# Performance work log

Measured on AMD Instinct MI355X. Metric: run time of the kernel, lower is better.

Reference implementation:

```python
import jax, jax.numpy as jnp
import numpy as np

B, T, F, H = 4096, 512, 16, 256
OUTPUT_LEN = 64


def setup_inputs() -> dict:
    key = jax.random.key(0)
    ks = jax.random.split(key, 9)
    s = 1.0 / np.sqrt(H)  # pytorch LSTM default init scale
    return {
        "x": jax.random.normal(ks[0], (B, T, F), jnp.float32),
        # encoder LSTM (single layer). b = b_ih + b_hh combined.
        "enc_Wih": jax.random.uniform(ks[1], (4 * H, F), jnp.float32, -s, s),
        "enc_Whh": jax.random.uniform(ks[2], (4 * H, H), jnp.float32, -s, s),
        "enc_b": jax.random.uniform(ks[3], (4 * H,), jnp.float32, -s, s),
        # decoder LSTM, input size 1
        "dec_Wih": jax.random.uniform(ks[4], (4 * H, 1), jnp.float32, -s, s),
        "dec_Whh": jax.random.uniform(ks[5], (4 * H, H), jnp.float32, -s, s),
        "dec_b": jax.random.uniform(ks[6], (4 * H,), jnp.float32, -s, s),
        # output head Linear(H, 1)
        "Wout": jax.random.uniform(ks[7], (1, H), jnp.float32, -s, s),
        "bout": jax.random.uniform(ks[8], (1,), jnp.float32, -s, s),
    }


def _lstm_cell(h, c, x_t, Wih, Whh, b):
    # PyTorch gate order: i, f, g, o
    gates = x_t @ Wih.T + h @ Whh.T + b  # [B, 4H]
    i, f, g, o = jnp.split(gates, 4, axis=-1)
    c = jax.nn.sigmoid(f) * c + jax.nn.sigmoid(i) * jnp.tanh(g)
    h = jax.nn.sigmoid(o) * jnp.tanh(c)
    return h, c


def reference(x, enc_Wih, enc_Whh, enc_b, dec_Wih, dec_Whh, dec_b, Wout, bout):
    Bb = x.shape[0]
    Hh = enc_Whh.shape[1]
    h0 = jnp.zeros((Bb, Hh), x.dtype)
    c0 = jnp.zeros((Bb, Hh), x.dtype)

    def enc_step(carry, x_t):
        h, c = carry
        h, c = _lstm_cell(h, c, x_t, enc_Wih, enc_Whh, enc_b)
        return (h, c), None

    (h, c), _ = jax.lax.scan(enc_step, (h0, c0), jnp.swapaxes(x, 0, 1))

    def dec_step(carry, _):
        h, c, inp = carry  # inp: [B, 1]
        h, c = _lstm_cell(h, c, inp, dec_Wih, dec_Whh, dec_b)
        # dropout is identity in eval mode
        out = h @ Wout.T + bout  # [B, 1]
        return (h, c, out), out

    inp0 = jnp.zeros((Bb, 1), x.dtype)
    _, outs = jax.lax.scan(dec_step, (h, c, inp0), None, length=OUTPUT_LEN)
    # outs: [output_len, B, 1] -> [B, output_len, 1]
    return jnp.swapaxes(outs, 0, 1)
```

## Files before the change

### kernel.cpp

```cpp
#include <hip/hip_runtime.h>

#define TT 512
#define FF 16
#define HH 256
#define OUTLEN 64
#define NT 9
#define PITCH 296
#define ROWS 16
#define NBLK (4096/ROWS)
#define NFRAG (NT*16*4*64)

typedef _Float16 half8 __attribute__((ext_vector_type(8)));
typedef float f32x4 __attribute__((ext_vector_type(4)));

__device__ __forceinline__ float fsig(float x) {
  return __builtin_amdgcn_rcpf(1.0f + __expf(-x));
}
__device__ __forceinline__ float ftanh(float x) { return 2.0f * fsig(x + x) - 1.0f; }

__global__ void prep_kernel(const float* __restrict__ eWih, const float* __restrict__ eWhh,
                            const float* __restrict__ eb,  const float* __restrict__ dWih,
                            const float* __restrict__ dWhh, const float* __restrict__ db,
                            _Float16* __restrict__ E, _Float16* __restrict__ D) {
  int idx = blockIdx.x * 256 + threadIdx.x;
  if (idx >= NFRAG * 8) return;
  int j    = idx & 7;
  int lane = (idx >> 3) & 63;
  int rest = idx >> 9;
  int g    = rest & 3;
  int wv   = (rest >> 2) & 15;
  int kt   = rest >> 6;
  int col  = g * 256 + wv * 16 + (lane & 15);
  int k    = kt * 32 + (lane >> 4) * 8 + j;
  float ve = 0.f, vd = 0.f;
  if (k < HH)        { ve = eWhh[col * HH + k]; vd = dWhh[col * HH + k]; }
  else if (k == HH)  { ve = eb[col];            vd = db[col]; }
  else if (k <= 272) { ve = eWih[col * FF + (k - 257)]; if (k == 257) vd = dWih[col]; }
  E[idx] = (_Float16)ve;
  D[idx] = (_Float16)vd;
}

__device__ __forceinline__ void fill_bf(half8 (&bf)[2][4], const half8* __restrict__ strm) {
#pragma unroll
  for (int g = 0; g < 4; ++g) bf[0][g] = strm[0 * 4096 + g * 64];
#pragma unroll
  for (int g = 0; g < 4; ++g) bf[1][g] = strm[1 * 4096 + g * 64];
}

__device__ __forceinline__ void fill_pk(half8 (&pk)[3][4], const half8* __restrict__ pp) {
#pragma unroll
  for (int i = 0; i < 3; ++i)
#pragma unroll
    for (int g = 0; g < 4; ++g) pk[i][g] = pp[i * 4096 + g * 64];
}

#define PIN_PK(pk)                                                   \
  _Pragma("unroll")                                                  \
  for (int _i = 0; _i < 3; ++_i)                                     \
    _Pragma("unroll")                                                \
    for (int _g = 0; _g < 4; ++_g)                                   \
      asm volatile("" : "+v"(pk[_i][_g]));

__device__ __forceinline__ void mfma_step(const _Float16* __restrict__ uHp,
                                          const _Float16* __restrict__ uLp,
                                          const half8* __restrict__ Btp,
                                          const half8* __restrict__ strm,
                                          const half8 (&pk)[3][4],
                                          half8 (&bf)[2][4],
                                          f32x4 (&acc)[4]) {
#pragma unroll
  for (int g = 0; g < 4; ++g) acc[g] = (f32x4){0.f, 0.f, 0.f, 0.f};

#pragma unroll
  for (int s = 0; s < 2; ++s) {
    half8 AH = *(const half8*)(uHp + (5 + s) * 32);
    half8 AL = *(const half8*)(uLp + (5 + s) * 32);
#pragma unroll
    for (int g = 0; g < 4; ++g) acc[g] = __builtin_amdgcn_mfma_f32_16x16x32_f16(AH, bf[s][g], acc[g], 0, 0, 0);
#pragma unroll
    for (int g = 0; g < 4; ++g) acc[g] = __builtin_amdgcn_mfma_f32_16x16x32_f16(AL, bf[s][g], acc[g], 0, 0, 0);
    {
      const half8* rp = strm + (s + 2) * 4096;
#pragma unroll
      for (int g = 0; g < 4; ++g) bf[s][g] = rp[g * 64];
    }
  }

#pragma unroll
  for (int kt = 0; kt < 2; ++kt) {
    half8 b[4];
#pragma unroll
    for (int g = 0; g < 4; ++g) b[g] = Btp[kt * 4096 + g * 64];
    half8 AH = *(const half8*)(uHp + kt * 32);
    half8 AL = *(const half8*)(uLp + kt * 32);
#pragma unroll
    for (int g = 0; g < 4; ++g) acc[g] = __builtin_amdgcn_mfma_f32_16x16x32_f16(AH, b[g], acc[g], 0, 0, 0);
#pragma unroll
    for (int g = 0; g < 4; ++g) acc[g] = __builtin_amdgcn_mfma_f32_16x16x32_f16(AL, b[g], acc[g], 0, 0, 0);
  }

#pragma unroll
  for (int s = 2; s < 4; ++s) {
    half8 AH = *(const half8*)(uHp + (5 + s) * 32);
    half8 AL = *(const half8*)(uLp + (5 + s) * 32);
#pragma unroll
    for (int g = 0; g < 4; ++g) acc[g] = __builtin_amdgcn_mfma_f32_16x16x32_f16(AH, bf[s - 2][g], acc[g], 0, 0, 0);
#pragma unroll
    for (int g = 0; g < 4; ++g) acc[g] = __builtin_amdgcn_mfma_f32_16x16x32_f16(AL, bf[s - 2][g], acc[g], 0, 0, 0);
    {
      const half8* rp = strm + (s - 2) * 4096;
#pragma unroll
      for (int g = 0; g < 4; ++g) bf[s - 2][g] = rp[g * 64];
    }
  }

#pragma unroll
  for (int i = 0; i < 3; ++i) {
    half8 AH = *(const half8*)(uHp + (2 + i) * 32);
    half8 AL = *(const half8*)(uLp + (2 + i) * 32);
#pragma unroll
    for (int g = 0; g < 4; ++g) acc[g] = __builtin_amdgcn_mfma_f32_16x16x32_f16(AH, pk[i][g], acc[g], 0, 0, 0);
#pragma unroll
    for (int g = 0; g < 4; ++g) acc[g] = __builtin_amdgcn_mfma_f32_16x16x32_f16(AL, pk[i][g], acc[g], 0, 0, 0);
  }
}

__global__ __launch_bounds__(1024, 4) void seq2seq_kernel(
    const float* __restrict__ x,
    const _Float16* __restrict__ E, const _Float16* __restrict__ Dw,
    const float* __restrict__ Wout, const float* __restrict__ bout,
    float* __restrict__ out) {
  __shared__ _Float16 uH[ROWS * PITCH];
  __shared__ _Float16 uL[ROWS * PITCH];
  __shared__ half8 Bt[2 * 16 * 4 * 64];
  __shared__ float red[ROWS * 16];

  const int tid  = threadIdx.x;
  const int w    = tid >> 6;
  const int lane = tid & 63;
  const int quad = lane >> 4;
  const int l15  = lane & 15;
  const int b0   = blockIdx.x * ROWS;
  const int unit = w * 16 + l15;

  const half8* E8 = (const half8*)E;
  const half8* D8 = (const half8*)Dw;

  for (int i = tid; i < ROWS * PITCH; i += 1024) { uH[i] = (_Float16)0.f; uL[i] = (_Float16)0.f; }
  for (int i = tid; i < 8192; i += 1024) Bt[i] = E8[i];
  __syncthreads();
  if (tid < ROWS) uH[tid * PITCH + 256] = (_Float16)1.0f;

  const _Float16* uHp = uH + l15 * PITCH + quad * 8;
  const _Float16* uLp = uL + l15 * PITCH + quad * 8;
  const half8* Btp  = Bt + w * 256 + lane;
  const half8* strm = E8 + 5 * 4096 + w * 256 + lane;

  float cc[4] = {0.f, 0.f, 0.f, 0.f};
  const float wou = Wout[unit];
  const float bo  = bout[0];
  const int   xr  = (tid >> 4) * PITCH + 257 + (tid & 15);
  const float* xp = x + ((long)(b0 + (tid >> 4)) * TT) * FF + (tid & 15);

  half8 pk[3][4];
  fill_pk(pk, E8 + 2 * 4096 + w * 256 + lane);
  half8 bf[2][4];
  fill_bf(bf, strm);

  float xv = (tid < 256) ? xp[0] : 0.f;
#pragma unroll 1
  for (int t = 0; t < TT; ++t) {
    PIN_PK(pk);
    if (tid < 256) {
      _Float16 hs = (_Float16)xv;
      uH[xr] = hs; uL[xr] = (_Float16)(xv - (float)hs);
      if (t + 1 < TT) xv = xp[(t + 1) * FF];
    }
    __syncthreads();

    f32x4 acc[4];
    mfma_step(uHp, uLp, Btp, strm, pk, bf, acc);
    __syncthreads();

#pragma unroll
    for (int rg = 0; rg < 4; ++rg) {
      float ig = fsig(acc[0][rg]);
      float fg = fsig(acc[1][rg]);
      float gg = ftanh(acc[2][rg]);
      float og = fsig(acc[3][rg]);
      cc[rg] = fg * cc[rg] + ig * gg;
      float hv = og * ftanh(cc[rg]);
      const int m = quad * 4 + rg;
      _Float16 hs = (_Float16)hv;
      uH[m * PITCH + unit] = hs;
      uL[m * PITCH + unit] = (_Float16)(hv - (float)hs);
    }
  }

  __syncthreads();
  for (int i = tid; i < 8192; i += 1024) Bt[i] = D8[i];
  strm = D8 + 5 * 4096 + w * 256 + lane;
  fill_pk(pk, D8 + 2 * 4096 + w * 256 + lane);
  fill_bf(bf, strm);
  if (tid < ROWS) { uH[tid * PITCH + 257] = (_Float16)0.f; uL[tid * PITCH + 257] = (_Float16)0.f; }

#pragma unroll 1
  for (int td = 0; td < OUTLEN; ++td) {
    PIN_PK(pk);
    __syncthreads();

    f32x4 acc[4];
    mfma_step(uHp, uLp, Btp, strm, pk, bf, acc);
    __syncthreads();

    float p[4];
#pragma unroll
    for (int rg = 0; rg < 4; ++rg) {
      float ig = fsig(acc[0][rg]);
      float fg = fsig(acc[1][rg]);
      float gg = ftanh(acc[2][rg]);
      float og = fsig(acc[3][rg]);
      cc[rg] = fg * cc[rg] + ig * gg;
      float hv = og * ftanh(cc[rg]);
      const int m = quad * 4 + rg;
      _Float16 hs = (_Float16)hv;
      uH[m * PITCH + unit] = hs;
      uL[m * PITCH + unit] = (_Float16)(hv - (float)hs);
      p[rg] = hv * wou;
    }
#pragma unroll
    for (int off = 1; off < 16; off <<= 1)
#pragma unroll
      for (int rg = 0; rg < 4; ++rg) p[rg] += __shfl_xor(p[rg], off, 64);
    if (l15 == 0) {
#pragma unroll
      for (int rg = 0; rg < 4; ++rg) red[(quad * 4 + rg) * 16 + w] = p[rg];
    }
    __syncthreads();
    if (tid < ROWS) {
      float s = bo;
#pragma unroll
      for (int u = 0; u < 16; ++u) s += red[tid * 16 + u];
      out[(long)(b0 + tid) * OUTLEN + td] = s;
      _Float16 hs = (_Float16)s;
      uH[tid * PITCH + 257] = hs;
      uL[tid * PITCH + 257] = (_Float16)(s - (float)hs);
    }
  }
}

extern "C" void kernel_launch(void* const* d_in, const int* in_sizes, int n_in,
                              void* d_out, int out_size, void* d_ws, size_t ws_size,
                              hipStream_t stream) {
  const float* x    = (const float*)d_in[0];
  const float* eWih = (const float*)d_in[1];
  const float* eWhh = (const float*)d_in[2];
  const float* eb   = (const float*)d_in[3];
  const float* dWih = (const float*)d_in[4];
  const float* dWhh = (const float*)d_in[5];
  const float* db   = (const float*)d_in[6];
  const float* Wout = (const float*)d_in[7];
  const float* bout = (const float*)d_in[8];
  float* out = (float*)d_out;

  _Float16* E  = (_Float16*)d_ws;
  _Float16* Dw = E + NFRAG * 8;

  prep_kernel<<<dim3((NFRAG * 8 + 255) / 256), dim3(256), 0, stream>>>(
      eWih, eWhh, eb, dWih, dWhh, db, E, Dw);
  seq2seq_kernel<<<dim3(NBLK), dim3(1024), 0, stream>>>(
      x, E, Dw, Wout, bout, out);
}
```

Measured before the change: 2.899 ms.

## Halve block to 512 threads with each wave computing two hidden-unit slices

Each block now runs 8 waves instead of 16, and each wave owns two 16-unit column slices. A-fragment loads from LDS are reused across twice as many MFMAs, and the pinned weight fragments double per wave. The weight-streaming schedule is reorganised around consume/refill helpers. This cuts barrier participants and shared-memory A traffic but raises register pressure and halves thread-level parallelism per block, with launch bounds changed to (512,2).

```diff
diff --git a/kernel.cpp b/kernel.cpp
--- a/kernel.cpp
+++ b/kernel.cpp
@@ -40,92 +40,103 @@
   D[idx] = (_Float16)vd;
 }
 
-__device__ __forceinline__ void fill_bf(half8 (&bf)[2][4], const half8* __restrict__ strm) {
-#pragma unroll
-  for (int g = 0; g < 4; ++g) bf[0][g] = strm[0 * 4096 + g * 64];
-#pragma unroll
-  for (int g = 0; g < 4; ++g) bf[1][g] = strm[1 * 4096 + g * 64];
-}
-
-__device__ __forceinline__ void fill_pk(half8 (&pk)[3][4], const half8* __restrict__ pp) {
+__device__ __forceinline__ void refill_bf(half8 (&bf)[2][4], const half8* __restrict__ rp) {
+#pragma unroll
+  for (int s = 0; s < 2; ++s)
+#pragma unroll
+    for (int g = 0; g < 4; ++g) bf[s][g] = rp[s * 256 + g * 64];
+}
+
+__device__ __forceinline__ void fill_pk(half8 (&pk)[3][2][4], const half8* __restrict__ pp) {
 #pragma unroll
   for (int i = 0; i < 3; ++i)
 #pragma unroll
-    for (int g = 0; g < 4; ++g) pk[i][g] = pp[i * 4096 + g * 64];
+    for (int s = 0; s < 2; ++s)
+#pragma unroll
+      for (int g = 0; g < 4; ++g) pk[i][s][g] = pp[i * 4096 + s * 256 + g * 64];
 }
 
 #define PIN_PK(pk)                                                   \
   _Pragma("unroll")                                                  \
   for (int _i = 0; _i < 3; ++_i)                                     \
     _Pragma("unroll")                                                \
-    for (int _g = 0; _g < 4; ++_g)                                   \
-      asm volatile("" : "+v"(pk[_i][_g]));
+    for (int _s = 0; _s < 2; ++_s)                                   \
+      _Pragma("unroll")                                              \
+      for (int _g = 0; _g < 4; ++_g)                                 \
+        asm volatile("" : "+v"(pk[_i][_s][_g]));
+
+__device__ __forceinline__ void consume_bf(const _Float16* __restrict__ uHp,
+                                           const _Float16* __restrict__ uLp,
+                                           const int kt, const half8 (&bf)[2][4],
+                                           f32x4 (&acc)[2][4]) {
+  half8 AH = *(const half8*)(uHp + kt * 32);
+  half8 AL = *(const half8*)(uLp + kt * 32);
+#pragma unroll
+  for (int s = 0; s < 2; ++s) {
+#pragma unroll
+    for (int g = 0; g < 4; ++g) acc[s][g] = __builtin_amdgcn_mfma_f32_16x16x32_f16(AH, bf[s][g], acc[s][g], 0, 0, 0);
+#pragma unroll
+    for (int g = 0; g < 4; ++g) acc[s][g] = __builtin_amdgcn_mfma_f32_16x16x32_f16(AL, bf[s][g], acc[s][g], 0, 0, 0);
+  }
+}
+
+__device__ __forceinline__ void consume_lds(const _Float16* __restrict__ uHp,
+                                            const _Float16* __restrict__ uLp,
+                                            const int kt, const half8* __restrict__ Btp,
+                                            f32x4 (&acc)[2][4]) {
+  half8 AH = *(const half8*)(uHp + kt * 32);
+  half8 AL = *(const half8*)(uLp + kt * 32);
+#pragma unroll
+  for (int s = 0; s < 2; ++s) {
+    half8 b[4];
+#pragma unroll
+    for (int g = 0; g < 4; ++g) b[g] = Btp[kt * 4096 + s * 256 + g * 64];
+#pragma unroll
+    for (int g = 0; g < 4; ++g) acc[s][g] = __builtin_amdgcn_mfma_f32_16x16x32_f16(AH, b[g], acc[s][g], 0, 0, 0);
+#pragma unroll
+    for (int g = 0; g < 4; ++g) acc[s][g] = __builtin_amdgcn_mfma_f32_16x16x32_f16(AL, b[g], acc[s][g], 0, 0, 0);
+  }
+}
+
+__device__ __forceinline__ void consume_pin(const _Float16* __restrict__ uHp,
+                                            const _Float16* __restrict__ uLp,
+                                            const int i, const half8 (&pk)[3][2][4],
+                                            f32x4 (&acc)[2][4]) {
+  half8 AH = *(const half8*)(uHp + (2 + i) * 32);
+  half8 AL = *(const half8*)(uLp + (2 + i) * 32);
+#pragma unroll
+  for (int s = 0; s < 2; ++s) {
+#pragma unroll
+    for (int g = 0; g < 4; ++g) acc[s][g] = __builtin_amdgcn_mfma_f32_16x16x32_f16(AH, pk[i][s][g], acc[s][g], 0, 0, 0);
+#pragma unroll
+    for (int g = 0; g < 4; ++g) acc[s][g] = __builtin_amdgcn_mfma_f32_16x16x32_f16(AL, pk[i][s][g], acc[s][g], 0, 0, 0);
+  }
+}
 
 __device__ __forceinline__ void mfma_step(const _Float16* __restrict__ uHp,
                                           const _Float16* __restrict__ uLp,
                                           const half8* __restrict__ Btp,
                                           const half8* __restrict__ strm,
-                                          const half8 (&pk)[3][4],
+                                          const half8 (&pk)[3][2][4],
                                           half8 (&bf)[2][4],
-                                          f32x4 (&acc)[4]) {
-#pragma unroll
-  for (int g = 0; g < 4; ++g) acc[g] = (f32x4){0.f, 0.f, 0.f, 0.f};
-
-#pragma unroll
-  for (int s = 0; s < 2; ++s) {
-    half8 AH = *(const half8*)(uHp + (5 + s) * 32);
-    half8 AL = *(const half8*)(uLp + (5 + s) * 32);
-#pragma unroll
-    for (int g = 0; g < 4; ++g) acc[g] = __builtin_amdgcn_mfma_f32_16x16x32_f16(AH, bf[s][g], acc[g], 0, 0, 0);
-#pragma unroll
-    for (int g = 0; g < 4; ++g) acc[g] = __builtin_amdgcn_mfma_f32_16x16x32_f16(AL, bf[s][g], acc[g], 0, 0, 0);
-    {
-      const half8* rp = strm + (s + 2) * 4096;
-#pragma unroll
-      for (int g = 0; g < 4; ++g) bf[s][g] = rp[g * 64];
-    }
-  }
-
-#pragma unroll
-  for (int kt = 0; kt < 2; ++kt) {
-    half8 b[4];
-#pragma unroll
-    for (int g = 0; g < 4; ++g) b[g] = Btp[kt * 4096 + g * 64];
-    half8 AH = *(const half8*)(uHp + kt * 32);
-    half8 AL = *(const half8*)(uLp + kt * 32);
-#pragma unroll
-    for (int g = 0; g < 4; ++g) acc[g] = __builtin_amdgcn_mfma_f32_16x16x32_f16(AH, b[g], acc[g], 0, 0, 0);
-#pragma unroll
-    for (int g = 0; g < 4; ++g) acc[g] = __builtin_amdgcn_mfma_f32_16x16x32_f16(AL, b[g], acc[g], 0, 0, 0);
-  }
-
-#pragma unroll
-  for (int s = 2; s < 4; ++s) {
-    half8 AH = *(const half8*)(uHp + (5 + s) * 32);
-    half8 AL = *(const half8*)(uLp + (5 + s) * 32);
-#pragma unroll
-    for (int g = 0; g < 4; ++g) acc[g] = __builtin_amdgcn_mfma_f32_16x16x32_f16(AH, bf[s - 2][g], acc[g], 0, 0, 0);
-#pragma unroll
-    for (int g = 0; g < 4; ++g) acc[g] = __builtin_amdgcn_mfma_f32_16x16x32_f16(AL, bf[s - 2][g], acc[g], 0, 0, 0);
-    {
-      const half8* rp = strm + (s - 2) * 4096;
-#pragma unroll
-      for (int g = 0; g < 4; ++g) bf[s - 2][g] = rp[g * 64];
-    }
-  }
-
-#pragma unroll
-  for (int i = 0; i < 3; ++i) {
-    half8 AH = *(const half8*)(uHp + (2 + i) * 32);
-    half8 AL = *(const half8*)(uLp + (2 + i) * 32);
-#pragma unroll
-    for (int g = 0; g < 4; ++g) acc[g] = __builtin_amdgcn_mfma_f32_16x16x32_f16(AH, pk[i][g], acc[g], 0, 0, 0);
-#pragma unroll
-    for (int g = 0; g < 4; ++g) acc[g] = __builtin_amdgcn_mfma_f32_16x16x32_f16(AL, pk[i][g], acc[g], 0, 0, 0);
-  }
-}
-
-__global__ __launch_bounds__(1024, 4) void seq2seq_kernel(
+                                          f32x4 (&acc)[2][4]) {
+#pragma unroll
+  for (int s = 0; s < 2; ++s)
+#pragma unroll
+    for (int g = 0; g < 4; ++g) acc[s][g] = (f32x4){0.f, 0.f, 0.f, 0.f};
+
+  consume_bf(uHp, uLp, 5, bf, acc);  refill_bf(bf, strm + 1 * 4096);
+  consume_lds(uHp, uLp, 0, Btp, acc);
+  consume_bf(uHp, uLp, 6, bf, acc);  refill_bf(bf, strm + 2 * 4096);
+  consume_lds(uHp, uLp, 1, Btp, acc);
+  consume_bf(uHp, uLp, 7, bf, acc);  refill_bf(bf, strm + 3 * 4096);
+  consume_pin(uHp, uLp, 0, pk, acc);
+  consume_pin(uHp, uLp, 1, pk, acc);
+  consume_bf(uHp, uLp, 8, bf, acc);  refill_bf(bf, strm);
+  consume_pin(uHp, uLp, 2, pk, acc);
+}
+
+__global__ __launch_bounds__(512, 2) void seq2seq_kernel(
     const float* __restrict__ x,
     const _Float16* __restrict__ E, const _Float16* __restrict__ Dw,
     const float* __restrict__ Wout, const float* __restrict__ bout,
@@ -141,31 +152,32 @@
   const int quad = lane >> 4;
   const int l15  = lane & 15;
   const int b0   = blockIdx.x * ROWS;
-  const int unit = w * 16 + l15;
 
   const half8* E8 = (const half8*)E;
   const half8* D8 = (const half8*)Dw;
 
-  for (int i = tid; i < ROWS * PITCH; i += 1024) { uH[i] = (_Float16)0.f; uL[i] = (_Float16)0.f; }
-  for (int i = tid; i < 8192; i += 1024) Bt[i] = E8[i];
+  for (int i = tid; i < ROWS * PITCH; i += 512) { uH[i] = (_Float16)0.f; uL[i] = (_Float16)0.f; }
+  for (int i = tid; i < 8192; i += 512) Bt[i] = E8[i];
   __syncthreads();
   if (tid < ROWS) uH[tid * PITCH + 256] = (_Float16)1.0f;
 
   const _Float16* uHp = uH + l15 * PITCH + quad * 8;
   const _Float16* uLp = uL + l15 * PITCH + quad * 8;
-  const half8* Btp  = Bt + w * 256 + lane;
-  const half8* strm = E8 + 5 * 4096 + w * 256 + lane;
-
-  float cc[4] = {0.f, 0.f, 0.f, 0.f};
-  const float wou = Wout[unit];
+  const half8* Btp  = Bt + (2 * w) * 256 + lane;
+  const half8* strm = E8 + 5 * 4096 + (2 * w) * 256 + lane;
+
+  float cc[2][4] = {{0.f, 0.f, 0.f, 0.f}, {0.f, 0.f, 0.f, 0.f}};
+  float wou[2];
+  wou[0] = Wout[(2 * w) * 16 + l15];
+  wou[1] = Wout[(2 * w + 1) * 16 + l15];
   const float bo  = bout[0];
   const int   xr  = (tid >> 4) * PITCH + 257 + (tid & 15);
   const float* xp = x + ((long)(b0 + (tid >> 4)) * TT) * FF + (tid & 15);
 
-  half8 pk[3][4];
-  fill_pk(pk, E8 + 2 * 4096 + w * 256 + lane);
+  half8 pk[3][2][4];
+  fill_pk(pk, E8 + 2 * 4096 + (2 * w) * 256 + lane);
   half8 bf[2][4];
-  fill_bf(bf, strm);
+  refill_bf(bf, strm);
 
   float xv = (tid < 256) ? xp[0] : 0.f;
 #pragma unroll 1
@@ -178,30 +190,34 @@
     }
     __syncthreads();
 
-    f32x4 acc[4];
+    f32x4 acc[2][4];
     mfma_step(uHp, uLp, Btp, strm, pk, bf, acc);
     __syncthreads();
 
 #pragma unroll
-    for (int rg = 0; rg < 4; ++rg) {
-      float ig = fsig(acc[0][rg]);
-      float fg = fsig(acc[1][rg]);
-      float gg = ftanh(acc[2][rg]);
-      float og = fsig(acc[3][rg]);
-      cc[rg] = fg * cc[rg] + ig * gg;
-      float hv = og * ftanh(cc[rg]);
-      const int m = quad * 4 + rg;
-      _Float16 hs = (_Float16)hv;
-      uH[m * PITCH + unit] = hs;
-      uL[m * PITCH + unit] = (_Float16)(hv - (float)hs);
+    for (int s = 0; s < 2; ++s) {
+      const int unit = (2 * w + s) * 16 + l15;
+#pragma unroll
+      for (int rg = 0; rg < 4; ++rg) {
+        float ig = fsig(acc[s][0][rg]);
+        float fg = fsig(acc[s][1][rg]);
+        float gg = ftanh(acc[s][2][rg]);
+        float og = fsig(acc[s][3][rg]);
+        cc[s][rg] = fg * cc[s][rg] + ig * gg;
+        float hv = og * ftanh(cc[s][rg]);
+        const int m = quad * 4 + rg;
+        _Float16 hs = (_Float16)hv;
+        uH[m * PITCH + unit] = hs;
+        uL[m * PITCH + unit] = (_Float16)(hv - (float)hs);
+      }
     }
   }
 
   __syncthreads();
-  for (int i = tid; i < 8192; i += 1024) Bt[i] = D8[i];
-  strm = D8 + 5 * 4096 + w * 256 + lane;
-  fill_pk(pk, D8 + 2 * 4096 + w * 256 + lane);
-  fill_bf(bf, strm);
+  for (int i = tid; i < 8192; i += 512) Bt[i] = D8[i];
+  strm = D8 + 5 * 4096 + (2 * w) * 256 + lane;
+  fill_pk(pk, D8 + 2 * 4096 + (2 * w) * 256 + lane);
+  refill_bf(bf, strm);
   if (tid < ROWS) { uH[tid * PITCH + 257] = (_Float16)0.f; uL[tid * PITCH + 257] = (_Float16)0.f; }
 
 #pragma unroll 1
@@ -209,32 +225,40 @@
     PIN_PK(pk);
     __syncthreads();
 
-    f32x4 acc[4];
+    f32x4 acc[2][4];
     mfma_step(uHp, uLp, Btp, strm, pk, bf, acc);
     __syncthreads();
 
-    float p[4];
-#pragma unroll
-    for (int rg = 0; rg < 4; ++rg) {
-      float ig = fsig(acc[0][rg]);
-      float fg = fsig(acc[1][rg]);
-      float gg = ftanh(acc[2][rg]);
-      float og = fsig(acc[3][rg]);
-      cc[rg] = fg * cc[rg] + ig * gg;
-      float hv = og * ftanh(cc[rg]);
-      const int m = quad * 4 + rg;
-      _Float16 hs = (_Float16)hv;
-      uH[m * PITCH + unit] = hs;
-      uL[m * PITCH + unit] = (_Float16)(hv - (float)hs);
-      p[rg] = hv * wou;
+    float p[2][4];
+#pragma unroll
+    for (int s = 0; s < 2; ++s) {
+      const int unit = (2 * w + s) * 16 + l15;
+#pragma unroll
+      for (int rg = 0; rg < 4; ++rg) {
+        float ig = fsig(acc[s][0][rg]);
+        float fg = fsig(acc[s][1][rg]);
+        float gg = ftanh(acc[s][2][rg]);
+        float og = fsig(acc[s][3][rg]);
+        cc[s][rg] = fg * cc[s][rg] + ig * gg;
+        float hv = og * ftanh(cc[s][rg]);
+        const int m = quad * 4 + rg;
+        _Float16 hs = (_Float16)hv;
+        uH[m * PITCH + unit] = hs;
+        uL[m * PITCH + unit] = (_Float16)(hv - (float)hs);
+        p[s][rg] = hv * wou[s];
+      }
     }
 #pragma unroll
     for (int off = 1; off < 16; off <<= 1)
 #pragma unroll
-      for (int rg = 0; rg < 4; ++rg) p[rg] += __shfl_xor(p[rg], off, 64);
+      for (int s = 0; s < 2; ++s)
+#pragma unroll
+        for (int rg = 0; rg < 4; ++rg) p[s][rg] += __shfl_xor(p[s][rg], off, 64);
     if (l15 == 0) {
 #pragma unroll
-      for (int rg = 0; rg < 4; ++rg) red[(quad * 4 + rg) * 16 + w] = p[rg];
+      for (int s = 0; s < 2; ++s)
+#pragma unroll
+        for (int rg = 0; rg < 4; ++rg) red[(quad * 4 + rg) * 16 + 2 * w + s] = p[s][rg];
     }
     __syncthreads();
     if (tid < ROWS) {
@@ -268,6 +292,6 @@
 
   prep_kernel<<<dim3((NFRAG * 8 + 255) / 256), dim3(256), 0, stream>>>(
       eWih, eWhh, eb, dWih, dWhh, db, E, Dw);
-  seq2seq_kernel<<<dim3(NBLK), dim3(1024), 0, stream>>>(
+  seq2seq_kernel<<<dim3(NBLK), dim3(512), 0, stream>>>(
       x, E, Dw, Wout, bout, out);
 }
```

Result: faster. 2.688 ms (-7.3%).
